# Kernel optimization log

Measured on AMD Instinct MI355X. Metric: run time of the kernel, lower is better.

The kernel has to match this reference:

```python
import jax, jax.numpy as jnp
import numpy as np

VF = 3          # vote_factor
GRID = 0.1      # grid_size
P = 4           # padded per-group capacity (stands in for data-dependent max group size)
RATIO_MAX = 5   # original drops groups needing repeat ratio > 5
EPS = 1e-5
SHIFT, BASE = 512, 1024  # 3D->1D hash (int32-safe: BASE**3 < 2**31)


def _bn_relu(x, gamma, beta):
    # BatchNorm1d in train mode over the token (batch) axis; conv input is (N, C, 1)
    m = x.mean(axis=0)
    v = jnp.mean((x - m) ** 2, axis=0)  # biased variance, as torch BN uses for normalization
    return jax.nn.relu((x - m) * jax.lax.rsqrt(v + EPS) * gamma + beta)


def _one_sample(idv, cov, ftv, W1, b1, g1, be1, W2, b2, g2, be2, W3, b3):
    N, C = ftv.shape
    V = N * VF
    # conv1x1 stack == per-token linear layers
    h = _bn_relu(ftv @ W1.T + b1, g1, be1)
    h = _bn_relu(h @ W2.T + b2, g2, be2)
    log = (h @ W3.T + b3).reshape(N, VF, 3 + C)
    off3 = log[:, :, :3]                                  # (N, VF, 3)
    coor = (cov[:, None, :] + off3).reshape(V, 3)
    grid_res = (off3 / GRID).astype(jnp.int32)            # trunc toward zero, like .int()
    ind = (idv[:, None, :] + grid_res).reshape(V, 3)
    # Degenerate inner-dict loop (tensor keys hash by identity): every vote's feature
    # offset becomes offset[n][VF-1] * 3 / VF  (len(key)==3, idx stale at VF-1)
    feat_off = log[:, VF - 1, 3:] * (3.0 / VF)            # (N, C)
    feat = jnp.broadcast_to((ftv + feat_off)[:, None, :], (N, VF, C)).reshape(V, C)

    # group votes by quantized 3D index (tuple-key dict -> hash + unique + segment ops)
    hc = jnp.clip(ind, -SHIFT, SHIFT - 1) + SHIFT
    keys = (hc[:, 0] * BASE + hc[:, 1]) * BASE + hc[:, 2]  # (V,) int32
    _, inv = jnp.unique(keys, size=V, fill_value=-1, return_inverse=True)
    inv = inv.reshape(-1)
    ones = jnp.ones((V,), jnp.int32)
    counts = jax.ops.segment_sum(ones, inv, num_segments=V)          # group sizes
    order = jnp.argsort(inv)                                          # votes sorted by group
    starts = jnp.cumsum(counts) - counts
    first = jax.ops.segment_min(jnp.arange(V, dtype=jnp.int32), inv, num_segments=V)
    first = jnp.where(counts > 0, first, 0)
    ind_buf = jnp.where((counts > 0)[:, None], ind[first], 0).astype(jnp.int32)

    cnt_safe = jnp.maximum(counts, 1)
    p = jnp.arange(P, dtype=jnp.int32)
    src_pos = starts[:, None] + (p[None, :] % cnt_safe[:, None])      # (V, P) repeat-fill
    src = order[src_pos]
    valid = (counts > 0) & (counts * RATIO_MAX >= P)                  # ceil(P/cnt) <= 5
    coor_buf = jnp.where(valid[:, None, None], coor[src], 0.0)        # (V, P, 3)
    feat_buf = jnp.where(valid[:, None, None], feat[src], 0.0)        # (V, P, C)
    return ind_buf, coor_buf, feat_buf, valid


def setup_inputs() -> dict:
    key = jax.random.key(0)
    ks = jax.random.split(key, 12)
    B, N, C = 2, 16384, 128
    s = 1.0 / np.sqrt(C)
    return {
        "ID": jax.random.randint(ks[0], (B, N, 3), 0, 100, dtype=jnp.int32),
        "CO": jax.random.normal(ks[1], (B, N, 3), jnp.float32),
        "FT": jax.random.normal(ks[2], (B, N, C), jnp.float32),
        "W1": jax.random.normal(ks[3], (C, C), jnp.float32) * s,
        "b1": jnp.zeros((C,), jnp.float32),
        "g1": 1.0 + 0.1 * jax.random.normal(ks[4], (C,), jnp.float32),
        "be1": 0.1 * jax.random.normal(ks[5], (C,), jnp.float32),
        "W2": jax.random.normal(ks[6], (C, C), jnp.float32) * s,
        "b2": jnp.zeros((C,), jnp.float32),
        "g2": 1.0 + 0.1 * jax.random.normal(ks[7], (C,), jnp.float32),
        "be2": 0.1 * jax.random.normal(ks[8], (C,), jnp.float32),
        "W3": jax.random.normal(ks[9], ((3 + C) * VF, C), jnp.float32) * s,
        "b3": 0.01 * jax.random.normal(ks[10], ((3 + C) * VF,), jnp.float32),
    }


def reference(ID, CO, FT, W1, b1, g1, be1, W2, b2, g2, be2, W3, b3):
    outs = [_one_sample(ID[i], CO[i], FT[i], W1, b1, g1, be1, W2, b2, g2, be2, W3, b3)
            for i in range(ID.shape[0])]  # small fixed batch loop
    ind_buf = jnp.stack([o[0] for o in outs])
    coor_buf = jnp.stack([o[1] for o in outs])
    feat_buf = jnp.stack([o[2] for o in outs])
    mask = jnp.stack([o[3] for o in outs])
    return ind_buf, coor_buf, feat_buf, mask
```

## Files before the change

kernel.cpp:

```cpp
#include <hip/hip_runtime.h>

constexpr int Bn = 2;
constexpr int Nn = 16384;
constexpr int Cc = 128;
constexpr int VFh = 3;
constexpr int Vv = Nn * VFh;
constexpr int Pp = 4;
constexpr int LDc = 144;
constexpr int SB = 96;

constexpr size_t IND0  = 0;
constexpr size_t COOR0 = (size_t)Bn * Vv * 3;
constexpr size_t FEAT0 = COOR0 + (size_t)Bn * Vv * Pp * 3;
constexpr size_t MASK0 = FEAT0 + (size_t)Bn * Vv * Pp * Cc;

template<int JMAX, bool BN, bool COMPACT>
__global__ __launch_bounds__(256) void gemm_t(
    const float* __restrict__ A, const float* __restrict__ W,
    const float* __restrict__ bias, const float* __restrict__ ss,
    float* __restrict__ out, int ldo, int nRB)
{
    constexpr int BNT = JMAX * 16;
    __shared__ float As[64 * 36];
    __shared__ float Ws[BNT * 36];

    int bid = blockIdx.x;
    int s = bid / nRB, rb = bid % nRB;
    const float* Ag = A + (size_t)s * Nn * Cc + (size_t)rb * 64 * Cc;
    float* outg = out + (size_t)s * Nn * ldo + (size_t)rb * 64 * ldo;
    const float* sp = nullptr;
    if constexpr (BN) sp = ss + (size_t)s * 2 * Cc;

    int t = threadIdx.x, tx = t & 15, ty = t >> 4;

    float acc[4][JMAX];
    #pragma unroll
    for (int i = 0; i < 4; ++i)
        #pragma unroll
        for (int j = 0; j < JMAX; ++j) acc[i][j] = 0.f;

    for (int stage = 0; stage < 4; ++stage) {
        int k0 = stage * 32;
        if (stage) __syncthreads();
        #pragma unroll
        for (int r = 0; r < 2; ++r) {
            int idx = r * 256 + t;
            int row = idx >> 3, c4 = (idx & 7) * 4;
            float4 v = *(const float4*)(Ag + (size_t)row * Cc + k0 + c4);
            if constexpr (BN) {
                int ch = k0 + c4;
                v.x = fmaxf(0.f, fmaf(v.x, sp[ch + 0], sp[Cc + ch + 0]));
                v.y = fmaxf(0.f, fmaf(v.y, sp[ch + 1], sp[Cc + ch + 1]));
                v.z = fmaxf(0.f, fmaf(v.z, sp[ch + 2], sp[Cc + ch + 2]));
                v.w = fmaxf(0.f, fmaf(v.w, sp[ch + 3], sp[Cc + ch + 3]));
            }
            *(float4*)&As[row * 36 + c4] = v;
        }
        for (int idx = t; idx < BNT * 8; idx += 256) {
            int row = idx >> 3, c4 = (idx & 7) * 4;
            float4 v = make_float4(0.f, 0.f, 0.f, 0.f);
            bool ok = true;
            if constexpr (COMPACT) ok = (row < 137);
            if (ok) {
                int wr = row;
                if constexpr (COMPACT) wr = (row < 9) ? (row / 3) * 131 + (row % 3) : row + 256;
                v = *(const float4*)(W + (size_t)wr * Cc + k0 + c4);
            }
            *(float4*)&Ws[row * 36 + c4] = v;
        }
        __syncthreads();
        #pragma unroll
        for (int k4 = 0; k4 < 8; ++k4) {
            int k = k4 * 4;
            float4 av[4];
            #pragma unroll
            for (int i = 0; i < 4; ++i) av[i] = *(const float4*)&As[(i * 16 + ty) * 36 + k];
            #pragma unroll
            for (int j = 0; j < JMAX; ++j) {
                float4 wv = *(const float4*)&Ws[(j * 16 + tx) * 36 + k];
                #pragma unroll
                for (int i = 0; i < 4; ++i) {
                    float a0 = acc[i][j];
                    a0 = fmaf(av[i].x, wv.x, a0);
                    a0 = fmaf(av[i].y, wv.y, a0);
                    a0 = fmaf(av[i].z, wv.z, a0);
                    a0 = fmaf(av[i].w, wv.w, a0);
                    acc[i][j] = a0;
                }
            }
        }
    }
    #pragma unroll
    for (int j = 0; j < JMAX; ++j) {
        int col = j * 16 + tx;
        bool ok = true;
        if constexpr (COMPACT) ok = (col < 137);
        if (ok) {
            int br = col;
            if constexpr (COMPACT) br = (col < 9) ? (col / 3) * 131 + (col % 3) : col + 256;
            float bv = bias[br];
            #pragma unroll
            for (int i = 0; i < 4; ++i)
                outg[(size_t)(i * 16 + ty) * ldo + col] = acc[i][j] + bv;
        }
    }
}

__global__ void colstats(const float* __restrict__ Y, float* __restrict__ part)
{
    int blk = blockIdx.x;
    int s = blk >> 6, b = blk & 63;
    const float* Yp = Y + (size_t)s * Nn * Cc + (size_t)b * 256 * Cc;
    int c = threadIdx.x;
    float sm = 0.f, sq = 0.f;
    for (int r = 0; r < 256; ++r) {
        float v = Yp[(size_t)r * Cc + c];
        sm += v; sq += v * v;
    }
    float* pp = part + ((size_t)s * 64 + b) * 2 * Cc;
    pp[c] = sm;
    pp[Cc + c] = sq;
}

__global__ void bnfinalize(const float* __restrict__ part, const float* __restrict__ g,
                           const float* __restrict__ be, float* __restrict__ ss)
{
    int s = blockIdx.x, c = threadIdx.x;
    const float* pp = part + (size_t)s * 64 * 2 * Cc;
    float sm = 0.f, sq = 0.f;
    for (int b = 0; b < 64; ++b) {
        sm += pp[(size_t)b * 2 * Cc + c];
        sq += pp[(size_t)b * 2 * Cc + Cc + c];
    }
    float m   = sm / (float)Nn;
    float var = sq / (float)Nn - m * m;
    float inv = 1.0f / sqrtf(var + 1e-5f);
    float sc  = g[c] * inv;
    ss[(size_t)s * 2 * Cc + c]      = sc;
    ss[(size_t)s * 2 * Cc + Cc + c] = be[c] - m * sc;
}

__global__ void zerok(uint4* __restrict__ p)
{
    p[(size_t)blockIdx.x * 256 + threadIdx.x] = make_uint4(0, 0, 0, 0);
}

__global__ void prep(const float* __restrict__ LOGc, const float* __restrict__ FT,
                     const float* __restrict__ CO, const int* __restrict__ ID,
                     float* __restrict__ coor, int* __restrict__ indb,
                     float* __restrict__ featb, unsigned* __restrict__ keys,
                     unsigned* __restrict__ idx0, unsigned* __restrict__ histA)
{
    int blk = blockIdx.x;
    int s = blk >> 14, n = blk & 16383;
    const float* Lr = LOGc + ((size_t)s * Nn + n) * LDc;
    int t = threadIdx.x;
    featb[((size_t)s * Nn + n) * Cc + t] =
        FT[((size_t)s * Nn + n) * Cc + t] + Lr[9 + t];
    if (t < 3) {
        int j = t;
        float o0 = Lr[j * 3 + 0], o1 = Lr[j * 3 + 1], o2 = Lr[j * 3 + 2];
        int v = n * 3 + j;
        size_t vb = (size_t)s * Vv + v;
        const float* co = CO + ((size_t)s * Nn + n) * 3;
        coor[vb * 3 + 0] = co[0] + o0;
        coor[vb * 3 + 1] = co[1] + o1;
        coor[vb * 3 + 2] = co[2] + o2;
        const int* id = ID + ((size_t)s * Nn + n) * 3;
        int gi0 = (int)(o0 / 0.1f), gi1 = (int)(o1 / 0.1f), gi2 = (int)(o2 / 0.1f);
        int i0 = id[0] + gi0, i1 = id[1] + gi1, i2 = id[2] + gi2;
        indb[vb * 3 + 0] = i0; indb[vb * 3 + 1] = i1; indb[vb * 3 + 2] = i2;
        int h0 = min(max(i0, -512), 511) + 512;
        int h1 = min(max(i1, -512), 511) + 512;
        int h2 = min(max(i2, -512), 511) + 512;
        unsigned key = ((unsigned)h0 * 1024u + (unsigned)h1) * 1024u + (unsigned)h2;
        keys[vb] = key;
        idx0[vb] = (unsigned)v;
        atomicAdd(&histA[(size_t)s * SB * 1024 + (size_t)(v >> 9) * 1024 + (key & 1023u)], 1u);
    }
}

__global__ __launch_bounds__(1024) void scank(unsigned* __restrict__ h,
                                              unsigned* __restrict__ other,
                                              unsigned* __restrict__ BB, int zeroOther)
{
    int s = blockIdx.x, d = threadIdx.x;
    unsigned* hp = h + (size_t)s * SB * 1024;
    unsigned run = 0;
    for (int b = 0; b < SB; ++b) {
        unsigned v = hp[(size_t)b * 1024 + d];
        hp[(size_t)b * 1024 + d] = run;
        run += v;
    }
    __shared__ unsigned sh[1024];
    sh[d] = run;
    __syncthreads();
    for (int off = 1; off < 1024; off <<= 1) {
        unsigned add = (d >= off) ? sh[d - off] : 0u;
        __syncthreads();
        sh[d] += add;
        __syncthreads();
    }
    BB[s * 1024 + d] = sh[d] - run;
    if (zeroOther) {
        unsigned* op = other + (size_t)s * SB * 1024;
        for (int b = 0; b < SB; ++b) op[(size_t)b * 1024 + d] = 0u;
    }
}

template<int PASS>
__global__ __launch_bounds__(512) void scatterk(
    const unsigned* __restrict__ kIn, const unsigned* __restrict__ iIn,
    unsigned* __restrict__ kOut, unsigned* __restrict__ iOut,
    const unsigned* __restrict__ hpref, const unsigned* __restrict__ BB,
    unsigned* __restrict__ nextH)
{
    __shared__ unsigned hl[1024];
    int t = threadIdx.x;
    hl[t] = 0u; hl[512 + t] = 0u;
    __syncthreads();
    int blk = blockIdx.x;
    int s = blk / SB, b = blk % SB;
    size_t base = (size_t)s * Vv + (size_t)b * 512 + t;
    unsigned key = kIn[base], idx = iIn[base];
    unsigned d = (key >> (PASS * 10)) & 1023u;
    unsigned long long m = ~0ull;
    #pragma unroll
    for (int bit = 0; bit < 10; ++bit) {
        bool bb = (d >> bit) & 1u;
        unsigned long long bal = __ballot(bb);
        m &= bb ? bal : ~bal;
    }
    int lane = t & 63, wid = t >> 6;
    int lanesBelow = __popcll(m & ((1ull << lane) - 1ull));
    int cnt = __popcll(m);
    int leader = __ffsll((unsigned long long)m) - 1;
    unsigned basec = 0;
    for (int w = 0; w < 8; ++w) {
        if (wid == w) {
            basec = hl[d];
            if (lane == leader) hl[d] = basec + (unsigned)cnt;
        }
        __syncthreads();
    }
    unsigned dest = BB[s * 1024 + (int)d]
                  + hpref[(size_t)s * SB * 1024 + (size_t)b * 1024 + d]
                  + basec + (unsigned)lanesBelow;
    kOut[(size_t)s * Vv + dest] = key;
    iOut[(size_t)s * Vv + dest] = idx;
    if constexpr (PASS < 2) {
        unsigned d2 = (key >> ((PASS + 1) * 10)) & 1023u;
        atomicAdd(&nextH[(size_t)s * SB * 1024 + (size_t)(dest >> 9) * 1024 + d2], 1u);
    }
}

__global__ __launch_bounds__(512) void headsct(const unsigned* __restrict__ skeys,
                                               unsigned* __restrict__ hpart)
{
    int blk = blockIdx.x;
    int s = blk / SB, b = blk % SB;
    int i = b * 512 + threadIdx.x;
    size_t base = (size_t)s * Vv;
    unsigned k = skeys[base + i];
    bool head = (i == 0) || (skeys[base + i - 1] != k);
    __shared__ unsigned wsum[8];
    unsigned long long bal = __ballot(head);
    int lane = threadIdx.x & 63, wid = threadIdx.x >> 6;
    if (lane == 0) wsum[wid] = (unsigned)__popcll(bal);
    __syncthreads();
    if (threadIdx.x == 0) {
        unsigned tot = 0;
        for (int w = 0; w < 8; ++w) tot += wsum[w];
        hpart[s * SB + b] = tot;
    }
}

__global__ __launch_bounds__(512) void ranksk(const unsigned* __restrict__ skeys,
                                              const unsigned* __restrict__ hpart,
                                              unsigned* __restrict__ start,
                                              unsigned* __restrict__ nu)
{
    int blk = blockIdx.x;
    int s = blk / SB, b = blk % SB;
    int t = threadIdx.x;
    __shared__ unsigned hp[SB];
    __shared__ unsigned pre[SB + 1];
    if (t < SB) hp[t] = hpart[s * SB + t];
    __syncthreads();
    if (t == 0) {
        unsigned run = 0;
        for (int i = 0; i < SB; ++i) { pre[i] = run; run += hp[i]; }
        pre[SB] = run;
    }
    __syncthreads();
    int i = b * 512 + t;
    size_t base = (size_t)s * Vv;
    unsigned k = skeys[base + i];
    bool head = (i == 0) || (skeys[base + i - 1] != k);
    unsigned long long bal = __ballot(head);
    int lane = t & 63, wid = t >> 6;
    __shared__ unsigned wsum[8];
    if (lane == 0) wsum[wid] = (unsigned)__popcll(bal);
    __syncthreads();
    unsigned wbase = 0;
    for (int w = 0; w < wid; ++w) wbase += wsum[w];
    unsigned lpre = (unsigned)__popcll(bal & ((1ull << lane) - 1ull));
    if (head)
        start[(size_t)s * (Vv + 1) + pre[b] + wbase + lpre] = (unsigned)i;
    if (b == 0 && t == 0) {
        nu[s] = pre[SB];
        start[(size_t)s * (Vv + 1) + pre[SB]] = (unsigned)Vv;
    }
}

__global__ __launch_bounds__(256) void outputk(
    const unsigned* __restrict__ sidx, const unsigned* __restrict__ start,
    const unsigned* __restrict__ nu, const int* __restrict__ indb,
    const float* __restrict__ coor, const float* __restrict__ featb,
    float* __restrict__ out)
{
    int wid = threadIdx.x >> 6, lane = threadIdx.x & 63;
    int g = blockIdx.x * 4 + wid;
    int s = g / Vv, u = g - s * Vv;
    size_t su = (size_t)s * Vv + u;
    bool valid = (unsigned)u < nu[s];
    float4* out4 = (float4*)out;
    int f = lane & 31, jlo = lane >> 5;
    if (valid) {
        const unsigned* st = start + (size_t)s * (Vv + 1);
        unsigned i0 = st[u], i1 = st[u + 1];
        unsigned c = i1 - i0;
        unsigned my = sidx[(size_t)s * Vv + i0 + ((unsigned)(lane & 3)) % c];
        unsigned sv[4];
        sv[0] = __shfl(my, 0); sv[1] = __shfl(my, 1);
        sv[2] = __shfl(my, 2); sv[3] = __shfl(my, 3);
        const float4* fb = (const float4*)(featb + (size_t)s * Nn * Cc);
        #pragma unroll
        for (int h = 0; h < 2; ++h) {
            int j = jlo + 2 * h;
            out4[(FEAT0 >> 2) + su * 128 + (size_t)j * 32 + f] =
                fb[(size_t)(sv[j] / 3) * 32 + f];
        }
        if (lane < 12)
            out[COOR0 + su * 12 + lane] =
                coor[((size_t)s * Vv + sv[lane / 3]) * 3 + lane % 3];
        else if (lane < 15)
            out[IND0 + su * 3 + (lane - 12)] =
                (float)indb[((size_t)s * Vv + sv[0]) * 3 + (lane - 12)];
        else if (lane == 15)
            out[MASK0 + su] = 1.f;
    } else {
        float4 z = make_float4(0.f, 0.f, 0.f, 0.f);
        #pragma unroll
        for (int h = 0; h < 2; ++h)
            out4[(FEAT0 >> 2) + su * 128 + (size_t)(jlo + 2 * h) * 32 + f] = z;
        if (lane < 12)       out[COOR0 + su * 12 + lane] = 0.f;
        else if (lane < 15)  out[IND0 + su * 3 + (lane - 12)] = 0.f;
        else if (lane == 15) out[MASK0 + su] = 0.f;
    }
}

extern "C" void kernel_launch(void* const* d_in, const int* in_sizes, int n_in,
                              void* d_out, int out_size, void* d_ws, size_t ws_size,
                              hipStream_t stream)
{
    const int*   ID  = (const int*)d_in[0];
    const float* CO  = (const float*)d_in[1];
    const float* FT  = (const float*)d_in[2];
    const float* W1  = (const float*)d_in[3];
    const float* b1  = (const float*)d_in[4];
    const float* g1  = (const float*)d_in[5];
    const float* be1 = (const float*)d_in[6];
    const float* W2  = (const float*)d_in[7];
    const float* b2  = (const float*)d_in[8];
    const float* g2  = (const float*)d_in[9];
    const float* be2 = (const float*)d_in[10];
    const float* W3  = (const float*)d_in[11];
    const float* b3  = (const float*)d_in[12];
    float* out = (float*)d_out;

    char* wsc = (char*)d_ws;
    size_t off = 0;
    auto alloc = [&](size_t elems) -> void* {
        void* p = wsc + off;
        off += ((elems * 4 + 255) & ~(size_t)255);
        return p;
    };
    float*    H1    = (float*)alloc((size_t)Bn * Nn * Cc);
    float*    H2    = (float*)alloc((size_t)Bn * Nn * Cc);
    float*    LOGc  = (float*)alloc((size_t)Bn * Nn * LDc);
    float*    PART  = (float*)alloc((size_t)Bn * 64 * 2 * Cc);
    float*    SS    = (float*)alloc((size_t)Bn * 2 * Cc);
    float*    COORb = (float*)alloc((size_t)Bn * Vv * 3);
    int*      INDB  = (int*)alloc((size_t)Bn * Vv * 3);
    float*    FEATB = (float*)alloc((size_t)Bn * Nn * Cc);
    unsigned* KA    = (unsigned*)alloc((size_t)Bn * Vv);
    unsigned* IA    = (unsigned*)alloc((size_t)Bn * Vv);
    unsigned* KB    = (unsigned*)alloc((size_t)Bn * Vv);
    unsigned* IB    = (unsigned*)alloc((size_t)Bn * Vv);
    unsigned* HA    = (unsigned*)alloc((size_t)Bn * SB * 1024);
    unsigned* HB    = (unsigned*)alloc((size_t)Bn * SB * 1024);
    unsigned* BBuf  = (unsigned*)alloc((size_t)Bn * 1024);
    unsigned* HP    = (unsigned*)alloc((size_t)Bn * SB);
    unsigned* NUp   = (unsigned*)alloc((size_t)Bn);
    unsigned* STp   = (unsigned*)alloc((size_t)Bn * (Vv + 1));
    (void)in_sizes; (void)n_in; (void)out_size; (void)ws_size;

    zerok<<<192, 256, 0, stream>>>((uint4*)HA);

    gemm_t<8, false, false><<<Bn * 256, 256, 0, stream>>>(FT, W1, b1, nullptr, H1, Cc, 256);
    colstats<<<Bn * 64, 128, 0, stream>>>(H1, PART);
    bnfinalize<<<Bn, 128, 0, stream>>>(PART, g1, be1, SS);
    gemm_t<8, true, false><<<Bn * 256, 256, 0, stream>>>(H1, W2, b2, SS, H2, Cc, 256);
    colstats<<<Bn * 64, 128, 0, stream>>>(H2, PART);
    bnfinalize<<<Bn, 128, 0, stream>>>(PART, g2, be2, SS);
    gemm_t<9, true, true><<<Bn * 256, 256, 0, stream>>>(H2, W3, b3, SS, LOGc, LDc, 256);

    prep<<<Bn * Nn, 128, 0, stream>>>(LOGc, FT, CO, ID, COORb, INDB, FEATB, KA, IA, HA);

    scank<<<Bn, 1024, 0, stream>>>(HA, HB, BBuf, 1);
    scatterk<0><<<Bn * SB, 512, 0, stream>>>(KA, IA, KB, IB, HA, BBuf, HB);
    scank<<<Bn, 1024, 0, stream>>>(HB, HA, BBuf, 1);
    scatterk<1><<<Bn * SB, 512, 0, stream>>>(KB, IB, KA, IA, HB, BBuf, HA);
    scank<<<Bn, 1024, 0, stream>>>(HA, HB, BBuf, 0);
    scatterk<2><<<Bn * SB, 512, 0, stream>>>(KA, IA, KB, IB, HA, BBuf, nullptr);

    headsct<<<Bn * SB, 512, 0, stream>>>(KB, HP);
    ranksk<<<Bn * SB, 512, 0, stream>>>(KB, HP, STp, NUp);

    outputk<<<Bn * Vv / 4, 256, 0, stream>>>(IB, STp, NUp, INDB, COORb, FEATB, out);
}
```

Measured before the change: 252.9 us.

## Fuse vote prep into third GEMM and fold histogram scans into radix scatter

The third GEMM now writes features, coordinates, voxel indices, hash keys and the first radix histogram directly from its epilogue. This removes the LOGc intermediate and the separate prep kernel. The radix sort drops the standalone scan kernels: each scatter block recomputes the global digit prefix from the histogram itself. Blocks are also enlarged to 1024 elements with per-wave local histograms, and three separate histogram buffers replace the re-zeroing ping-pong. The trade-off is redundant per-block prefix computation and more shared memory per scatter block.

```diff
diff --git a/kernel.cpp b/kernel.cpp
--- a/kernel.cpp
+++ b/kernel.cpp
@@ -3,41 +3,39 @@
 constexpr int Bn = 2;
 constexpr int Nn = 16384;
 constexpr int Cc = 128;
-constexpr int VFh = 3;
-constexpr int Vv = Nn * VFh;
+constexpr int Vv = Nn * 3;
 constexpr int Pp = 4;
-constexpr int LDc = 144;
-constexpr int SB = 96;
+constexpr int SB = 48;
+constexpr int HB = 96;
 
 constexpr size_t IND0  = 0;
 constexpr size_t COOR0 = (size_t)Bn * Vv * 3;
 constexpr size_t FEAT0 = COOR0 + (size_t)Bn * Vv * Pp * 3;
 constexpr size_t MASK0 = FEAT0 + (size_t)Bn * Vv * Pp * Cc;
 
-template<int JMAX, bool BN, bool COMPACT>
+template<bool BN>
 __global__ __launch_bounds__(256) void gemm_t(
     const float* __restrict__ A, const float* __restrict__ W,
     const float* __restrict__ bias, const float* __restrict__ ss,
-    float* __restrict__ out, int ldo, int nRB)
-{
-    constexpr int BNT = JMAX * 16;
+    float* __restrict__ out)
+{
     __shared__ float As[64 * 36];
-    __shared__ float Ws[BNT * 36];
+    __shared__ float Ws[128 * 36];
 
     int bid = blockIdx.x;
-    int s = bid / nRB, rb = bid % nRB;
+    int s = bid >> 8, rb = bid & 255;
     const float* Ag = A + (size_t)s * Nn * Cc + (size_t)rb * 64 * Cc;
-    float* outg = out + (size_t)s * Nn * ldo + (size_t)rb * 64 * ldo;
+    float* outg = out + (size_t)s * Nn * Cc + (size_t)rb * 64 * Cc;
     const float* sp = nullptr;
     if constexpr (BN) sp = ss + (size_t)s * 2 * Cc;
 
     int t = threadIdx.x, tx = t & 15, ty = t >> 4;
 
-    float acc[4][JMAX];
+    float acc[4][8];
     #pragma unroll
     for (int i = 0; i < 4; ++i)
         #pragma unroll
-        for (int j = 0; j < JMAX; ++j) acc[i][j] = 0.f;
+        for (int j = 0; j < 8; ++j) acc[i][j] = 0.f;
 
     for (int stage = 0; stage < 4; ++stage) {
         int k0 = stage * 32;
@@ -56,17 +54,11 @@
             }
             *(float4*)&As[row * 36 + c4] = v;
         }
-        for (int idx = t; idx < BNT * 8; idx += 256) {
+        #pragma unroll
+        for (int r = 0; r < 4; ++r) {
+            int idx = r * 256 + t;
             int row = idx >> 3, c4 = (idx & 7) * 4;
-            float4 v = make_float4(0.f, 0.f, 0.f, 0.f);
-            bool ok = true;
-            if constexpr (COMPACT) ok = (row < 137);
-            if (ok) {
-                int wr = row;
-                if constexpr (COMPACT) wr = (row < 9) ? (row / 3) * 131 + (row % 3) : row + 256;
-                v = *(const float4*)(W + (size_t)wr * Cc + k0 + c4);
-            }
-            *(float4*)&Ws[row * 36 + c4] = v;
+            *(float4*)&Ws[row * 36 + c4] = *(const float4*)(W + (size_t)row * Cc + k0 + c4);
         }
         __syncthreads();
         #pragma unroll
@@ -76,7 +68,7 @@
             #pragma unroll
             for (int i = 0; i < 4; ++i) av[i] = *(const float4*)&As[(i * 16 + ty) * 36 + k];
             #pragma unroll
-            for (int j = 0; j < JMAX; ++j) {
+            for (int j = 0; j < 8; ++j) {
                 float4 wv = *(const float4*)&Ws[(j * 16 + tx) * 36 + k];
                 #pragma unroll
                 for (int i = 0; i < 4; ++i) {
@@ -91,77 +83,119 @@
         }
     }
     #pragma unroll
-    for (int j = 0; j < JMAX; ++j) {
+    for (int j = 0; j < 8; ++j) {
         int col = j * 16 + tx;
-        bool ok = true;
-        if constexpr (COMPACT) ok = (col < 137);
-        if (ok) {
-            int br = col;
-            if constexpr (COMPACT) br = (col < 9) ? (col / 3) * 131 + (col % 3) : col + 256;
-            float bv = bias[br];
+        float bv = bias[col];
+        #pragma unroll
+        for (int i = 0; i < 4; ++i)
+            outg[(size_t)(i * 16 + ty) * Cc + col] = acc[i][j] + bv;
+    }
+}
+
+__global__ __launch_bounds__(256) void gemm3_fused(
+    const float* __restrict__ A, const float* __restrict__ W,
+    const float* __restrict__ bias, const float* __restrict__ ss,
+    const float* __restrict__ FT, const float* __restrict__ CO,
+    const int* __restrict__ ID,
+    float* __restrict__ featb, float* __restrict__ coor,
+    int* __restrict__ indb, unsigned* __restrict__ keys,
+    unsigned* __restrict__ idx0, unsigned* __restrict__ hist0)
+{
+    __shared__ float As[64 * 36];
+    __shared__ float Ws[144 * 36];
+
+    int bid = blockIdx.x;
+    int s = bid >> 8, rb = bid & 255;
+    const float* Ag = A + (size_t)s * Nn * Cc + (size_t)rb * 64 * Cc;
+    const float* sp = ss + (size_t)s * 2 * Cc;
+
+    int t = threadIdx.x, tx = t & 15, ty = t >> 4;
+
+    float acc[4][9];
+    #pragma unroll
+    for (int i = 0; i < 4; ++i)
+        #pragma unroll
+        for (int j = 0; j < 9; ++j) acc[i][j] = 0.f;
+
+    for (int stage = 0; stage < 4; ++stage) {
+        int k0 = stage * 32;
+        if (stage) __syncthreads();
+        #pragma unroll
+        for (int r = 0; r < 2; ++r) {
+            int idx = r * 256 + t;
+            int row = idx >> 3, c4 = (idx & 7) * 4;
+            float4 v = *(const float4*)(Ag + (size_t)row * Cc + k0 + c4);
+            int ch = k0 + c4;
+            v.x = fmaxf(0.f, fmaf(v.x, sp[ch + 0], sp[Cc + ch + 0]));
+            v.y = fmaxf(0.f, fmaf(v.y, sp[ch + 1], sp[Cc + ch + 1]));
+            v.z = fmaxf(0.f, fmaf(v.z, sp[ch + 2], sp[Cc + ch + 2]));
+            v.w = fmaxf(0.f, fmaf(v.w, sp[ch + 3], sp[Cc + ch + 3]));
+            *(float4*)&As[row * 36 + c4] = v;
+        }
+        for (int idx = t; idx < 144 * 8; idx += 256) {
+            int row = idx >> 3, c4 = (idx & 7) * 4;
+            float4 v = make_float4(0.f, 0.f, 0.f, 0.f);
+            if (row < 137) {
+                int wr = (row < 9) ? (row / 3) * 131 + (row % 3) : row + 256;
+                v = *(const float4*)(W + (size_t)wr * Cc + k0 + c4);
+            }
+            *(float4*)&Ws[row * 36 + c4] = v;
+        }
+        __syncthreads();
+        #pragma unroll
+        for (int k4 = 0; k4 < 8; ++k4) {
+            int k = k4 * 4;
+            float4 av[4];
+            #pragma unroll
+            for (int i = 0; i < 4; ++i) av[i] = *(const float4*)&As[(i * 16 + ty) * 36 + k];
+            #pragma unroll
+            for (int j = 0; j < 9; ++j) {
+                float4 wv = *(const float4*)&Ws[(j * 16 + tx) * 36 + k];
+                #pragma unroll
+                for (int i = 0; i < 4; ++i) {
+                    float a0 = acc[i][j];
+                    a0 = fmaf(av[i].x, wv.x, a0);
+                    a0 = fmaf(av[i].y, wv.y, a0);
+                    a0 = fmaf(av[i].z, wv.z, a0);
+                    a0 = fmaf(av[i].w, wv.w, a0);
+                    acc[i][j] = a0;
+                }
+            }
+        }
+    }
+
+    __syncthreads();
+    __shared__ float L9[64 * 12];
+    int n0 = rb * 64;
+    const float* FTg = FT + ((size_t)s * Nn + n0) * Cc;
+    float* FBg = featb + ((size_t)s * Nn + n0) * Cc;
+    #pragma unroll
+    for (int j = 0; j < 9; ++j) {
+        int col = j * 16 + tx;
+        if (col < 9) {
+            float bv = bias[(col / 3) * 131 + col % 3];
             #pragma unroll
             for (int i = 0; i < 4; ++i)
-                outg[(size_t)(i * 16 + ty) * ldo + col] = acc[i][j] + bv;
-        }
-    }
-}
-
-__global__ void colstats(const float* __restrict__ Y, float* __restrict__ part)
-{
-    int blk = blockIdx.x;
-    int s = blk >> 6, b = blk & 63;
-    const float* Yp = Y + (size_t)s * Nn * Cc + (size_t)b * 256 * Cc;
-    int c = threadIdx.x;
-    float sm = 0.f, sq = 0.f;
-    for (int r = 0; r < 256; ++r) {
-        float v = Yp[(size_t)r * Cc + c];
-        sm += v; sq += v * v;
-    }
-    float* pp = part + ((size_t)s * 64 + b) * 2 * Cc;
-    pp[c] = sm;
-    pp[Cc + c] = sq;
-}
-
-__global__ void bnfinalize(const float* __restrict__ part, const float* __restrict__ g,
-                           const float* __restrict__ be, float* __restrict__ ss)
-{
-    int s = blockIdx.x, c = threadIdx.x;
-    const float* pp = part + (size_t)s * 64 * 2 * Cc;
-    float sm = 0.f, sq = 0.f;
-    for (int b = 0; b < 64; ++b) {
-        sm += pp[(size_t)b * 2 * Cc + c];
-        sq += pp[(size_t)b * 2 * Cc + Cc + c];
-    }
-    float m   = sm / (float)Nn;
-    float var = sq / (float)Nn - m * m;
-    float inv = 1.0f / sqrtf(var + 1e-5f);
-    float sc  = g[c] * inv;
-    ss[(size_t)s * 2 * Cc + c]      = sc;
-    ss[(size_t)s * 2 * Cc + Cc + c] = be[c] - m * sc;
-}
-
-__global__ void zerok(uint4* __restrict__ p)
-{
-    p[(size_t)blockIdx.x * 256 + threadIdx.x] = make_uint4(0, 0, 0, 0);
-}
-
-__global__ void prep(const float* __restrict__ LOGc, const float* __restrict__ FT,
-                     const float* __restrict__ CO, const int* __restrict__ ID,
-                     float* __restrict__ coor, int* __restrict__ indb,
-                     float* __restrict__ featb, unsigned* __restrict__ keys,
-                     unsigned* __restrict__ idx0, unsigned* __restrict__ histA)
-{
-    int blk = blockIdx.x;
-    int s = blk >> 14, n = blk & 16383;
-    const float* Lr = LOGc + ((size_t)s * Nn + n) * LDc;
-    int t = threadIdx.x;
-    featb[((size_t)s * Nn + n) * Cc + t] =
-        FT[((size_t)s * Nn + n) * Cc + t] + Lr[9 + t];
-    if (t < 3) {
-        int j = t;
-        float o0 = Lr[j * 3 + 0], o1 = Lr[j * 3 + 1], o2 = Lr[j * 3 + 2];
-        int v = n * 3 + j;
+                L9[(i * 16 + ty) * 12 + col] = acc[i][j] + bv;
+        } else if (col < 137) {
+            int ch = col - 9;
+            float bv = bias[col + 256];
+            #pragma unroll
+            for (int i = 0; i < 4; ++i) {
+                int row = i * 16 + ty;
+                float lg = acc[i][j] + bv;
+                FBg[(size_t)row * Cc + ch] = FTg[(size_t)row * Cc + ch] + lg;
+            }
+        }
+    }
+    __syncthreads();
+    if (t < 192) {
+        int row = t / 3, jv = t - row * 3;
+        int n = n0 + row, v = n * 3 + jv;
         size_t vb = (size_t)s * Vv + v;
+        float o0 = L9[row * 12 + jv * 3 + 0];
+        float o1 = L9[row * 12 + jv * 3 + 1];
+        float o2 = L9[row * 12 + jv * 3 + 2];
         const float* co = CO + ((size_t)s * Nn + n) * 3;
         coor[vb * 3 + 0] = co[0] + o0;
         coor[vb * 3 + 1] = co[1] + o1;
@@ -176,81 +210,125 @@
         unsigned key = ((unsigned)h0 * 1024u + (unsigned)h1) * 1024u + (unsigned)h2;
         keys[vb] = key;
         idx0[vb] = (unsigned)v;
-        atomicAdd(&histA[(size_t)s * SB * 1024 + (size_t)(v >> 9) * 1024 + (key & 1023u)], 1u);
-    }
-}
-
-__global__ __launch_bounds__(1024) void scank(unsigned* __restrict__ h,
-                                              unsigned* __restrict__ other,
-                                              unsigned* __restrict__ BB, int zeroOther)
-{
-    int s = blockIdx.x, d = threadIdx.x;
-    unsigned* hp = h + (size_t)s * SB * 1024;
-    unsigned run = 0;
-    for (int b = 0; b < SB; ++b) {
-        unsigned v = hp[(size_t)b * 1024 + d];
-        hp[(size_t)b * 1024 + d] = run;
-        run += v;
-    }
-    __shared__ unsigned sh[1024];
-    sh[d] = run;
-    __syncthreads();
-    for (int off = 1; off < 1024; off <<= 1) {
-        unsigned add = (d >= off) ? sh[d - off] : 0u;
-        __syncthreads();
-        sh[d] += add;
-        __syncthreads();
-    }
-    BB[s * 1024 + d] = sh[d] - run;
-    if (zeroOther) {
-        unsigned* op = other + (size_t)s * SB * 1024;
-        for (int b = 0; b < SB; ++b) op[(size_t)b * 1024 + d] = 0u;
-    }
+        atomicAdd(&hist0[(size_t)s * SB * 1024 + (size_t)(v >> 10) * 1024 + (key & 1023u)], 1u);
+    }
+}
+
+__global__ void colstats(const float* __restrict__ Y, float* __restrict__ part)
+{
+    int blk = blockIdx.x;
+    int s = blk >> 6, b = blk & 63;
+    const float* Yp = Y + (size_t)s * Nn * Cc + (size_t)b * 256 * Cc;
+    int c = threadIdx.x;
+    float sm = 0.f, sq = 0.f;
+    for (int r = 0; r < 256; ++r) {
+        float v = Yp[(size_t)r * Cc + c];
+        sm += v; sq += v * v;
+    }
+    float* pp = part + ((size_t)s * 64 + b) * 2 * Cc;
+    pp[c] = sm;
+    pp[Cc + c] = sq;
+}
+
+__global__ void bnfinalize(const float* __restrict__ part, const float* __restrict__ g,
+                           const float* __restrict__ be, float* __restrict__ ss)
+{
+    int s = blockIdx.x, c = threadIdx.x;
+    const float* pp = part + (size_t)s * 64 * 2 * Cc;
+    float sm = 0.f, sq = 0.f;
+    for (int b = 0; b < 64; ++b) {
+        sm += pp[(size_t)b * 2 * Cc + c];
+        sq += pp[(size_t)b * 2 * Cc + Cc + c];
+    }
+    float m   = sm / (float)Nn;
+    float var = sq / (float)Nn - m * m;
+    float inv = 1.0f / sqrtf(var + 1e-5f);
+    float sc  = g[c] * inv;
+    ss[(size_t)s * 2 * Cc + c]      = sc;
+    ss[(size_t)s * 2 * Cc + Cc + c] = be[c] - m * sc;
+}
+
+__global__ void zerok(uint4* __restrict__ p)
+{
+    p[(size_t)blockIdx.x * 256 + threadIdx.x] = make_uint4(0, 0, 0, 0);
 }
 
 template<int PASS>
-__global__ __launch_bounds__(512) void scatterk(
+__global__ __launch_bounds__(512) void scat(
     const unsigned* __restrict__ kIn, const unsigned* __restrict__ iIn,
     unsigned* __restrict__ kOut, unsigned* __restrict__ iOut,
-    const unsigned* __restrict__ hpref, const unsigned* __restrict__ BB,
-    unsigned* __restrict__ nextH)
-{
-    __shared__ unsigned hl[1024];
-    int t = threadIdx.x;
-    hl[t] = 0u; hl[512 + t] = 0u;
-    __syncthreads();
-    int blk = blockIdx.x;
-    int s = blk / SB, b = blk % SB;
-    size_t base = (size_t)s * Vv + (size_t)b * 512 + t;
-    unsigned key = kIn[base], idx = iIn[base];
-    unsigned d = (key >> (PASS * 10)) & 1023u;
-    unsigned long long m = ~0ull;
-    #pragma unroll
-    for (int bit = 0; bit < 10; ++bit) {
-        bool bb = (d >> bit) & 1u;
-        unsigned long long bal = __ballot(bb);
-        m &= bb ? bal : ~bal;
-    }
-    int lane = t & 63, wid = t >> 6;
-    int lanesBelow = __popcll(m & ((1ull << lane) - 1ull));
-    int cnt = __popcll(m);
-    int leader = __ffsll((unsigned long long)m) - 1;
-    unsigned basec = 0;
-    for (int w = 0; w < 8; ++w) {
-        if (wid == w) {
-            basec = hl[d];
-            if (lane == leader) hl[d] = basec + (unsigned)cnt;
-        }
+    const unsigned* __restrict__ hist, unsigned* __restrict__ nextH)
+{
+    __shared__ unsigned hw[8 * 1024];
+    __shared__ unsigned tot[1024];
+    int t = threadIdx.x, lane = t & 63, w = t >> 6;
+    int blk = blockIdx.x, s = blk / SB, b = blk % SB;
+
+    #pragma unroll
+    for (int i = 0; i < 16; ++i) hw[w * 1024 + i * 64 + lane] = 0u;
+
+    const uint2* hs2 = (const uint2*)(hist + (size_t)s * SB * 1024);
+    int d0 = 2 * t, d1 = 2 * t + 1;
+    unsigned run0 = 0, run1 = 0, my0 = 0, my1 = 0;
+    for (int bb = 0; bb < SB; ++bb) {
+        uint2 v = hs2[bb * 512 + t];
+        if (bb == b) { my0 = run0; my1 = run1; }
+        run0 += v.x; run1 += v.y;
+    }
+    tot[d0] = run0; tot[d1] = run1;
+    __syncthreads();
+    for (int ofs = 1; ofs < 1024; ofs <<= 1) {
+        unsigned a0 = (d0 >= ofs) ? tot[d0 - ofs] : 0u;
+        unsigned a1 = (d1 >= ofs) ? tot[d1 - ofs] : 0u;
         __syncthreads();
-    }
-    unsigned dest = BB[s * 1024 + (int)d]
-                  + hpref[(size_t)s * SB * 1024 + (size_t)b * 1024 + d]
-                  + basec + (unsigned)lanesBelow;
-    kOut[(size_t)s * Vv + dest] = key;
-    iOut[(size_t)s * Vv + dest] = idx;
-    if constexpr (PASS < 2) {
-        unsigned d2 = (key >> ((PASS + 1) * 10)) & 1023u;
-        atomicAdd(&nextH[(size_t)s * SB * 1024 + (size_t)(dest >> 9) * 1024 + d2], 1u);
+        tot[d0] += a0; tot[d1] += a1;
+        __syncthreads();
+    }
+    tot[d0] = tot[d0] - run0 + my0;
+    tot[d1] = tot[d1] - run1 + my1;
+
+    size_t base = (size_t)s * Vv + (size_t)b * 1024;
+    unsigned keyE[2], idxE[2], rkE[2], dE[2];
+    #pragma unroll
+    for (int e = 0; e < 2; ++e) {
+        int pos = w * 128 + e * 64 + lane;
+        keyE[e] = kIn[base + pos];
+        idxE[e] = iIn[base + pos];
+        unsigned d = (keyE[e] >> (PASS * 10)) & 1023u;
+        dE[e] = d;
+        unsigned long long m = ~0ull;
+        #pragma unroll
+        for (int bit = 0; bit < 10; ++bit) {
+            bool bbit = (d >> bit) & 1u;
+            unsigned long long bal = __ballot(bbit);
+            m &= bbit ? bal : ~bal;
+        }
+        int lanesBelow = __popcll(m & ((1ull << lane) - 1ull));
+        int cnt = __popcll(m);
+        int leader = __ffsll((unsigned long long)m) - 1;
+        unsigned basec = hw[w * 1024 + d];
+        if (lane == leader) hw[w * 1024 + d] = basec + (unsigned)cnt;
+        rkE[e] = basec + (unsigned)lanesBelow;
+    }
+    __syncthreads();
+    {
+        unsigned r0 = 0, r1 = 0;
+        for (int ww = 0; ww < 8; ++ww) {
+            unsigned v0 = hw[ww * 1024 + d0], v1 = hw[ww * 1024 + d1];
+            hw[ww * 1024 + d0] = r0; hw[ww * 1024 + d1] = r1;
+            r0 += v0; r1 += v1;
+        }
+    }
+    __syncthreads();
+    #pragma unroll
+    for (int e = 0; e < 2; ++e) {
+        unsigned dest = tot[dE[e]] + hw[w * 1024 + dE[e]] + rkE[e];
+        kOut[(size_t)s * Vv + dest] = keyE[e];
+        iOut[(size_t)s * Vv + dest] = idxE[e];
+        if constexpr (PASS < 2) {
+            unsigned d2 = (keyE[e] >> ((PASS + 1) * 10)) & 1023u;
+            atomicAdd(&nextH[(size_t)s * SB * 1024 + (size_t)(dest >> 10) * 1024 + d2], 1u);
+        }
     }
 }
 
@@ -258,7 +336,7 @@
                                                unsigned* __restrict__ hpart)
 {
     int blk = blockIdx.x;
-    int s = blk / SB, b = blk % SB;
+    int s = blk / HB, b = blk % HB;
     int i = b * 512 + threadIdx.x;
     size_t base = (size_t)s * Vv;
     unsigned k = skeys[base + i];
@@ -271,7 +349,7 @@
     if (threadIdx.x == 0) {
         unsigned tot = 0;
         for (int w = 0; w < 8; ++w) tot += wsum[w];
-        hpart[s * SB + b] = tot;
+        hpart[s * HB + b] = tot;
     }
 }
 
@@ -281,16 +359,16 @@
                                               unsigned* __restrict__ nu)
 {
     int blk = blockIdx.x;
-    int s = blk / SB, b = blk % SB;
+    int s = blk / HB, b = blk % HB;
     int t = threadIdx.x;
-    __shared__ unsigned hp[SB];
-    __shared__ unsigned pre[SB + 1];
-    if (t < SB) hp[t] = hpart[s * SB + t];
+    __shared__ unsigned hp[HB];
+    __shared__ unsigned pre[HB + 1];
+    if (t < HB) hp[t] = hpart[s * HB + t];
     __syncthreads();
     if (t == 0) {
         unsigned run = 0;
-        for (int i = 0; i < SB; ++i) { pre[i] = run; run += hp[i]; }
-        pre[SB] = run;
+        for (int i = 0; i < HB; ++i) { pre[i] = run; run += hp[i]; }
+        pre[HB] = run;
     }
     __syncthreads();
     int i = b * 512 + t;
@@ -308,8 +386,8 @@
     if (head)
         start[(size_t)s * (Vv + 1) + pre[b] + wbase + lpre] = (unsigned)i;
     if (b == 0 && t == 0) {
-        nu[s] = pre[SB];
-        start[(size_t)s * (Vv + 1) + pre[SB]] = (unsigned)Vv;
+        nu[s] = pre[HB];
+        start[(size_t)s * (Vv + 1) + pre[HB]] = (unsigned)Vv;
     }
 }
 
@@ -386,9 +464,8 @@
         off += ((elems * 4 + 255) & ~(size_t)255);
         return p;
     };
-    float*    H1    = (float*)alloc((size_t)Bn * Nn * Cc);
-    float*    H2    = (float*)alloc((size_t)Bn * Nn * Cc);
-    float*    LOGc  = (float*)alloc((size_t)Bn * Nn * LDc);
+    float*    H1b   = (float*)alloc((size_t)Bn * Nn * Cc);
+    float*    H2b   = (float*)alloc((size_t)Bn * Nn * Cc);
     float*    PART  = (float*)alloc((size_t)Bn * 64 * 2 * Cc);
     float*    SS    = (float*)alloc((size_t)Bn * 2 * Cc);
     float*    COORb = (float*)alloc((size_t)Bn * Vv * 3);
@@ -398,35 +475,32 @@
     unsigned* IA    = (unsigned*)alloc((size_t)Bn * Vv);
     unsigned* KB    = (unsigned*)alloc((size_t)Bn * Vv);
     unsigned* IB    = (unsigned*)alloc((size_t)Bn * Vv);
-    unsigned* HA    = (unsigned*)alloc((size_t)Bn * SB * 1024);
-    unsigned* HB    = (unsigned*)alloc((size_t)Bn * SB * 1024);
-    unsigned* BBuf  = (unsigned*)alloc((size_t)Bn * 1024);
-    unsigned* HP    = (unsigned*)alloc((size_t)Bn * SB);
+    unsigned* H0h   = (unsigned*)alloc((size_t)Bn * SB * 1024);
+    unsigned* H1h   = (unsigned*)alloc((size_t)Bn * SB * 1024);
+    unsigned* H2h   = (unsigned*)alloc((size_t)Bn * SB * 1024);
+    unsigned* HP    = (unsigned*)alloc((size_t)Bn * HB);
     unsigned* NUp   = (unsigned*)alloc((size_t)Bn);
     unsigned* STp   = (unsigned*)alloc((size_t)Bn * (Vv + 1));
     (void)in_sizes; (void)n_in; (void)out_size; (void)ws_size;
 
-    zerok<<<192, 256, 0, stream>>>((uint4*)HA);
-
-    gemm_t<8, false, false><<<Bn * 256, 256, 0, stream>>>(FT, W1, b1, nullptr, H1, Cc, 256);
-    colstats<<<Bn * 64, 128, 0, stream>>>(H1, PART);
+    zerok<<<288, 256, 0, stream>>>((uint4*)H0h);
+
+    gemm_t<false><<<Bn * 256, 256, 0, stream>>>(FT, W1, b1, nullptr, H1b);
+    colstats<<<Bn * 64, 128, 0, stream>>>(H1b, PART);
     bnfinalize<<<Bn, 128, 0, stream>>>(PART, g1, be1, SS);
-    gemm_t<8, true, false><<<Bn * 256, 256, 0, stream>>>(H1, W2, b2, SS, H2, Cc, 256);
-    colstats<<<Bn * 64, 128, 0, stream>>>(H2, PART);
+    gemm_t<true><<<Bn * 256, 256, 0, stream>>>(H1b, W2, b2, SS, H2b);
+    colstats<<<Bn * 64, 128, 0, stream>>>(H2b, PART);
     bnfinalize<<<Bn, 128, 0, stream>>>(PART, g2, be2, SS);
-    gemm_t<9, true, true><<<Bn * 256, 256, 0, stream>>>(H2, W3, b3, SS, LOGc, LDc, 256);
-
-    prep<<<Bn * Nn, 128, 0, stream>>>(LOGc, FT, CO, ID, COORb, INDB, FEATB, KA, IA, HA);
-
-    scank<<<Bn, 1024, 0, stream>>>(HA, HB, BBuf, 1);
-    scatterk<0><<<Bn * SB, 512, 0, stream>>>(KA, IA, KB, IB, HA, BBuf, HB);
-    scank<<<Bn, 1024, 0, stream>>>(HB, HA, BBuf, 1);
-    scatterk<1><<<Bn * SB, 512, 0, stream>>>(KB, IB, KA, IA, HB, BBuf, HA);
-    scank<<<Bn, 1024, 0, stream>>>(HA, HB, BBuf, 0);
-    scatterk<2><<<Bn * SB, 512, 0, stream>>>(KA, IA, KB, IB, HA, BBuf, nullptr);
-
-    headsct<<<Bn * SB, 512, 0, stream>>>(KB, HP);
-    ranksk<<<Bn * SB, 512, 0, stream>>>(KB, HP, STp, NUp);
+
+    gemm3_fused<<<Bn * 256, 256, 0, stream>>>(H2b, W3, b3, SS, FT, CO, ID,
+                                              FEATB, COORb, INDB, KA, IA, H0h);
+
+    scat<0><<<Bn * SB, 512, 0, stream>>>(KA, IA, KB, IB, H0h, H1h);
+    scat<1><<<Bn * SB, 512, 0, stream>>>(KB, IB, KA, IA, H1h, H2h);
+    scat<2><<<Bn * SB, 512, 0, stream>>>(KA, IA, KB, IB, H2h, nullptr);
+
+    headsct<<<Bn * HB, 512, 0, stream>>>(KB, HP);
+    ranksk<<<Bn * HB, 512, 0, stream>>>(KB, HP, STp, NUp);
 
     outputk<<<Bn * Vv / 4, 256, 0, stream>>>(IB, STp, NUp, INDB, COORb, FEATB, out);
 }
```

New measurement: 213.3 us (median of 2 runs). 1.19x faster.
